# Performance work log

Hardware: AMD Instinct MI355X
Metric: run time of the kernel (lower is better)

## Reference

```python
import jax, jax.numpy as jnp
import numpy as np

B = 4
DIM = 512          # d_model
L = 4096           # n_tokens
D_STATE = 16
D_CONV = 4
EXPAND = 2
D_INNER = EXPAND * DIM          # 1024
DT_RANK = (DIM + 15) // 16      # ceil(dim/16) = 32
EPS = 1e-5


def setup_inputs() -> dict:
    key = jax.random.key(0)
    ks = jax.random.split(key, 8)
    s = 0.02
    A_log = jnp.log(jnp.tile(jnp.arange(1.0, D_STATE + 1.0, dtype=jnp.float32), (D_INNER, 1)))
    return {
        "x": jax.random.normal(ks[0], (B, DIM, L), jnp.float32),
        "ln_w": jnp.ones((DIM,), jnp.float32),
        "ln_b": jnp.zeros((DIM,), jnp.float32),
        "W_in": jax.random.normal(ks[1], (2 * D_INNER, DIM), jnp.float32) * s,
        "conv_w": jax.random.normal(ks[2], (D_INNER, 1, D_CONV), jnp.float32) * s,
        "conv_b": jnp.zeros((D_INNER,), jnp.float32),
        "W_xproj": jax.random.normal(ks[3], (DT_RANK + 2 * D_STATE, D_INNER), jnp.float32) * s,
        "W_dt": jax.random.normal(ks[4], (D_INNER, DT_RANK), jnp.float32) * s,
        "b_dt": jax.random.normal(ks[5], (D_INNER,), jnp.float32) * 0.1,
        "A_log": A_log,
        "D": jnp.ones((D_INNER,), jnp.float32),
        "W_out": jax.random.normal(ks[6], (DIM, D_INNER), jnp.float32) * s,
    }


def reference(x, ln_w, ln_b, W_in, conv_w, conv_b, W_xproj, W_dt, b_dt, A_log, D, W_out):
    Bsz = x.shape[0]
    # [B, d_model, L] -> [B, L, d_model]
    xt = jnp.swapaxes(x, 1, 2)
    # LayerNorm
    mu = jnp.mean(xt, axis=-1, keepdims=True)
    var = jnp.mean(jnp.square(xt - mu), axis=-1, keepdims=True)
    xn = (xt - mu) * jax.lax.rsqrt(var + EPS) * ln_w + ln_b
    # in_proj -> x, z branches
    xz = xn @ W_in.T                       # [B, L, 2*d_inner]
    xin, z = jnp.split(xz, 2, axis=-1)
    # causal depthwise conv1d (torch pads d_conv-1 both sides then truncates to L)
    xc = jnp.swapaxes(xin, 1, 2)           # [B, d_inner, L]
    xc = jax.lax.conv_general_dilated(
        xc, conv_w, window_strides=(1,), padding=[(D_CONV - 1, 0)],
        dimension_numbers=("NCH", "OIH", "NCH"), feature_group_count=D_INNER)
    xc = xc + conv_b[None, :, None]
    u = jax.nn.silu(jnp.swapaxes(xc, 1, 2))  # [B, L, d_inner]
    # input-dependent SSM parameters
    dbl = u @ W_xproj.T                    # [B, L, dt_rank + 2*d_state]
    dt = dbl[..., :DT_RANK]
    Bm = dbl[..., DT_RANK:DT_RANK + D_STATE]
    Cm = dbl[..., DT_RANK + D_STATE:]
    delta = jax.nn.softplus(dt @ W_dt.T + b_dt)  # [B, L, d_inner]
    A = -jnp.exp(A_log)                    # [d_inner, d_state]

    def step(h, inp):
        d_t, b_t, c_t, u_t = inp           # [B,di], [B,ds], [B,ds], [B,di]
        dA = jnp.exp(d_t[..., None] * A)   # [B, di, ds]
        h = dA * h + (d_t * u_t)[..., None] * b_t[:, None, :]
        y = jnp.einsum("bds,bs->bd", h, c_t)
        return h, y

    h0 = jnp.zeros((Bsz, D_INNER, D_STATE), x.dtype)
    xs = (jnp.swapaxes(delta, 0, 1), jnp.swapaxes(Bm, 0, 1),
          jnp.swapaxes(Cm, 0, 1), jnp.swapaxes(u, 0, 1))
    _, ys = jax.lax.scan(step, h0, xs)     # ys: [L, B, d_inner]
    y = jnp.swapaxes(ys, 0, 1) + u * D
    y = y * jax.nn.silu(z)
    out = y @ W_out.T                      # [B, L, d_model]
    return jnp.swapaxes(out, 1, 2)         # [B, d_model, L]
```

## Files before the change

### kernel.cpp

```cpp
#include <hip/hip_runtime.h>
#include <math.h>

#define Bsz 4
#define DIM 512
#define LEN 4096
#define DST 16
#define DIN 1024
#define NCH 64
#define CHL 64

typedef unsigned short ushort_t;
typedef unsigned int uint_t;
typedef __attribute__((ext_vector_type(8))) short short8;
typedef __attribute__((ext_vector_type(8))) unsigned short ushort8;
typedef __attribute__((ext_vector_type(8))) _Float16 half8;
typedef __attribute__((ext_vector_type(4))) float f32x4;

__device__ __forceinline__ float sigmoidf_(float x){ return 1.0f/(1.0f+__expf(-x)); }
__device__ __forceinline__ float bf2f(ushort_t u){ return __uint_as_float(((uint_t)u) << 16); }
__device__ __forceinline__ ushort_t f2bf(float f){
  uint_t x = __float_as_uint(f);
  uint_t r = (x + 0x7FFFu + ((x >> 16) & 1u)) >> 16;
  return (ushort_t)r;
}
__device__ __forceinline__ ushort_t f2h_bits(float f){
  _Float16 h = (_Float16)f;
  union { _Float16 h; ushort_t u; } v; v.h = h; return v.u;
}
__device__ __forceinline__ void gl2lds16(const void* g, void* l){
  __builtin_amdgcn_global_load_lds((const __attribute__((address_space(1))) void*)g,
                                   (__attribute__((address_space(3))) void*)l, 16, 0, 0);
}
#define POW_CHAIN(av, a1) \
  { float a2=a1*a1, a4=a2*a2, a8=a4*a4; \
    av[0]=a1; av[1]=a2; av[2]=a2*a1; av[3]=a4; \
    av[4]=a4*a1; av[5]=a4*a2; av[6]=a4*av[2]; av[7]=a8; \
    av[8]=a8*a1; av[9]=a8*a2; av[10]=a8*av[2]; av[11]=a8*a4; \
    av[12]=a8*av[4]; av[13]=a8*av[5]; av[14]=a8*av[6]; av[15]=a8*a8; }

__device__ __forceinline__ bool load_nA(const float* Alog, int d, float* nA){
  bool fast = true;
  #pragma unroll
  for(int s=0;s<DST;s++){
    float v = -__expf(Alog[d*DST+s]);
    float tgt = -(float)(s+1);
    if(fabsf(v - tgt) < 1e-4f*(float)(s+1)) v = tgt;
    else fast = false;
    nA[s] = v;
  }
  return fast;
}

__global__ __launch_bounds__(256) void ln_stats_k(const float* __restrict__ x,
                                                  float* __restrict__ mu, float* __restrict__ rs){
  int bid = blockIdx.x;
  int b = bid >> 6;
  int lg = bid & 63;
  int lane = threadIdx.x & 63;
  int g = threadIdx.x >> 6;
  int l = lg*64 + lane;
  const float* xb = x + (size_t)b*DIM*LEN + l;
  float s = 0.f, sq = 0.f;
  for(int d = g*128; d < g*128 + 128; ++d){
    float v = xb[(size_t)d*LEN];
    s += v; sq += v*v;
  }
  __shared__ float rsum[4][64], rsq[4][64];
  rsum[g][lane] = s; rsq[g][lane] = sq;
  __syncthreads();
  if(threadIdx.x < 64){
    float ts = 0.f, tq = 0.f;
    for(int gg=0; gg<4; ++gg){ ts += rsum[gg][lane]; tq += rsq[gg][lane]; }
    float m = ts * (1.0f/DIM);
    float var = tq * (1.0f/DIM) - m*m;
    mu[b*LEN + l] = m;
    rs[b*LEN + l] = rsqrtf(var + 1e-5f);
  }
}

__global__ __launch_bounds__(256) void wcvt_k(const float* __restrict__ Win,
    const float* __restrict__ Wout, const float* __restrict__ Wxp,
    ushort_t* __restrict__ Winb, ushort_t* __restrict__ Woutb, ushort_t* __restrict__ Wxpb){
  int i = blockIdx.x*256 + threadIdx.x;
  if(i < 1048576) Winb[i] = f2bf(Win[i]);
  else if(i < 1572864) Woutb[i-1048576] = f2bf(Wout[i-1048576]);
  else if(i < 1638400) Wxpb[i-1572864] = f2bf(Wxp[i-1572864]);
}

__global__ __launch_bounds__(256) void xnt_k(const float* __restrict__ x,
    const float* __restrict__ mu, const float* __restrict__ rs,
    const float* __restrict__ lnw, const float* __restrict__ lnb, ushort_t* __restrict__ xnT){
  __shared__ ushort_t t[64][72];
  int bid = blockIdx.x;
  int lt = bid & 63;
  int dt_ = (bid >> 6) & 7;
  int b = bid >> 9;
  int l0 = lt*64, d0 = dt_*64;
  int ll = threadIdx.x & 63;
  int dq = threadIdx.x >> 6;
  float mul_ = mu[b*LEN + l0 + ll], rsl = rs[b*LEN + l0 + ll];
  const float* xb = x + (size_t)b*DIM*LEN;
  #pragma unroll
  for(int i=0;i<16;i++){
    int d = d0 + dq*16 + i;
    float v = xb[(size_t)d*LEN + l0 + ll];
    t[ll][dq*16 + i] = f2bf((v - mul_)*rsl*lnw[d] + lnb[d]);
  }
  __syncthreads();
  int lr = threadIdx.x >> 2, seg = threadIdx.x & 3;
  ushort_t* dst = &xnT[(size_t)(b*LEN + l0 + lr)*DIM + d0 + seg*16];
  #pragma unroll
  for(int k=0;k<4;k++){
    ushort4 v = *(const ushort4*)&t[lr][seg*16 + k*4];
    *(ushort4*)&dst[k*4] = v;
  }
}

__global__ __launch_bounds__(256) void gemm1_mfma(const ushort_t* __restrict__ A,
    const ushort_t* __restrict__ Bw, _Float16* __restrict__ xin, ushort_t* __restrict__ sz){
  __shared__ __align__(16) ushort_t smem[2*16384];
  int tid = threadIdx.x;
  int wave = tid >> 6, lane = tid & 63;
  int flat = blockIdx.y * 16 + blockIdx.x;
  int orig = (flat & 7) * 256 + (flat >> 3);
  int n0 = (orig & 15) * 128;
  int m0 = (orig >> 4) * 128;
  int wm = (wave >> 1) * 64, wn = (wave & 1) * 64;
  int lm = lane & 15;
  int lk = lane >> 4;
  int sx = lm & 7;
  f32x4 zero4 = {0.f,0.f,0.f,0.f};
  f32x4 acc[4][4];
  #pragma unroll
  for(int i=0;i<4;i++)
    #pragma unroll
    for(int j=0;j<4;j++) acc[i][j] = zero4;
  #pragma unroll
  for(int i=0;i<4;i++){
    int c = i*256 + tid, r = c >> 3, kc = c & 7;
    int kg = kc ^ (r & 7);
    gl2lds16(&A [(size_t)(m0 + r)*512 + kg*8], &smem[c*8]);
    gl2lds16(&Bw[(size_t)(n0 + r)*512 + kg*8], &smem[8192 + c*8]);
  }
  int cur = 0;
  for(int t=0; t<8; ++t){
    if(t < 7){
      int k0n = (t+1)*64;
      ushort_t* Ad = &smem[(cur^1)*16384];
      ushort_t* Bd = &smem[(cur^1)*16384 + 8192];
      #pragma unroll
      for(int i=0;i<4;i++){
        int c = i*256 + tid, r = c >> 3, kc = c & 7;
        int kg = kc ^ (r & 7);
        gl2lds16(&A [(size_t)(m0 + r)*512 + k0n + kg*8], &Ad[c*8]);
        gl2lds16(&Bw[(size_t)(n0 + r)*512 + k0n + kg*8], &Bd[c*8]);
      }
      asm volatile("s_waitcnt vmcnt(8)" ::: "memory");
    } else {
      asm volatile("s_waitcnt vmcnt(0)" ::: "memory");
    }
    __builtin_amdgcn_sched_barrier(0);
    __builtin_amdgcn_s_barrier();
    const ushort_t* As = &smem[cur*16384];
    const ushort_t* Bs = &smem[cur*16384 + 8192];
    #pragma unroll
    for(int kk=0; kk<64; kk+=32){
      short8 af[4], bf[4];
      int ch = ((kk >> 3) + lk) ^ sx;
      #pragma unroll
      for(int i=0;i<4;i++){
        af[i] = *(const short8*)&As[(wm + i*16 + lm)*64 + ch*8];
        bf[i] = *(const short8*)&Bs[(wn + i*16 + lm)*64 + ch*8];
      }
      #pragma unroll
      for(int i=0;i<4;i++)
        #pragma unroll
        for(int j=0;j<4;j++)
          acc[i][j] = __builtin_amdgcn_mfma_f32_16x16x32_bf16(af[i], bf[j], acc[i][j], 0, 0, 0);
    }
    __builtin_amdgcn_s_barrier();
    cur ^= 1;
  }
  ushort_t* T = smem;
  bool is_z = (n0 >= 1024);
  #pragma unroll
  for(int i=0;i<4;i++)
    #pragma unroll
    for(int j=0;j<4;j++)
      #pragma unroll
      for(int r=0;r<4;r++){
        int ml = wm + i*16 + lk*4 + r;
        int nl = wn + j*16 + lm;
        float v = acc[i][j][r];
        T[ml*136 + nl] = is_z ? f2bf(v * sigmoidf_(v)) : f2h_bits(v);
      }
  __syncthreads();
  int rr = tid >> 4, cc = (tid & 15)*8;
  #pragma unroll
  for(int p=0;p<8;p++){
    int row = p*16 + rr;
    ushort8 v = *(const ushort8*)&T[row*136 + cc];
    if(!is_z) *(ushort8*)((ushort_t*)xin + (size_t)(m0+row)*DIN + n0 + cc) = v;
    else      *(ushort8*)&sz[(size_t)(m0+row)*DIN + (n0-1024) + cc] = v;
  }
}

__global__ __launch_bounds__(256) void conv_silu_k(const _Float16* __restrict__ xin,
    const float* __restrict__ cw, const float* __restrict__ cb, ushort_t* __restrict__ u){
  int idx = blockIdx.x*256 + threadIdx.x;
  int dg = idx & 127;
  int lc = (idx >> 7) & 511;
  int b  = idx >> 16;
  int d0 = dg*8;
  int l0 = lc*8;
  float bias[8];
  #pragma unroll
  for(int k=0;k<8;k+=4){
    float4 c4 = *(const float4*)&cb[d0+k];
    bias[k]=c4.x; bias[k+1]=c4.y; bias[k+2]=c4.z; bias[k+3]=c4.w;
  }
  float w[8][4];
  #pragma unroll
  for(int k=0;k<8;k++){
    float4 c4 = *(const float4*)&cw[(d0+k)*4];
    w[k][0]=c4.x; w[k][1]=c4.y; w[k][2]=c4.z; w[k][3]=c4.w;
  }
  const _Float16* base = xin + ((size_t)b*LEN)*DIN + d0;
  ushort_t* ub = u + ((size_t)b*LEN)*DIN + d0;
  float f0[8], f1[8], f2[8];
  if(lc > 0){
    half8 h0 = *(const half8*)&base[(size_t)(l0-3)*DIN];
    half8 h1 = *(const half8*)&base[(size_t)(l0-2)*DIN];
    half8 h2 = *(const half8*)&base[(size_t)(l0-1)*DIN];
    #pragma unroll
    for(int k=0;k<8;k++){ f0[k]=(float)h0[k]; f1[k]=(float)h1[k]; f2[k]=(float)h2[k]; }
  } else {
    #pragma unroll
    for(int k=0;k<8;k++){ f0[k]=0.f; f1[k]=0.f; f2[k]=0.f; }
  }
  #pragma unroll
  for(int t=0;t<8;t++){
    half8 xv = *(const half8*)&base[(size_t)(l0+t)*DIN];
    float f3[8];
    #pragma unroll
    for(int k=0;k<8;k++) f3[k] = (float)xv[k];
    short8 o;
    #pragma unroll
    for(int k=0;k<8;k++){
      float a = bias[k] + f0[k]*w[k][0] + f1[k]*w[k][1] + f2[k]*w[k][2] + f3[k]*w[k][3];
      float v = a * sigmoidf_(a);
      o[k] = (short)f2bf(v);
    }
    *(short8*)&ub[(size_t)(l0+t)*DIN] = o;
    #pragma unroll
    for(int k=0;k<8;k++){ f0[k]=f1[k]; f1[k]=f2[k]; f2[k]=f3[k]; }
  }
}

__global__ __launch_bounds__(256) void gemm2_mfma(const ushort_t* __restrict__ A,
    const ushort_t* __restrict__ Bw, float* __restrict__ dbl){
  __shared__ __align__(16) ushort_t smem[2*8192];
  int tid = threadIdx.x;
  int wave = tid >> 6, lane = tid & 63;
  int m0 = blockIdx.x * 64;
  int wm = (wave >> 1) * 32, wn = (wave & 1) * 32;
  int lm = lane & 15;
  int lk = lane >> 4;
  int sx = lm & 7;
  f32x4 zero4 = {0.f,0.f,0.f,0.f};
  f32x4 acc[2][2];
  #pragma unroll
  for(int i=0;i<2;i++){ acc[i][0] = zero4; acc[i][1] = zero4; }
  #pragma unroll
  for(int i=0;i<2;i++){
    int c = i*256 + tid, r = c >> 3, kc = c & 7;
    int kg = kc ^ (r & 7);
    gl2lds16(&A [(size_t)(m0 + r)*1024 + kg*8], &smem[c*8]);
    gl2lds16(&Bw[(size_t)r*1024 + kg*8], &smem[4096 + c*8]);
  }
  int cur = 0;
  for(int t=0; t<16; ++t){
    if(t < 15){
      int k0n = (t+1)*64;
      ushort_t* Ad = &smem[(cur^1)*8192];
      ushort_t* Bd = &smem[(cur^1)*8192 + 4096];
      #pragma unroll
      for(int i=0;i<2;i++){
        int c = i*256 + tid, r = c >> 3, kc = c & 7;
        int kg = kc ^ (r & 7);
        gl2lds16(&A [(size_t)(m0 + r)*1024 + k0n + kg*8], &Ad[c*8]);
        gl2lds16(&Bw[(size_t)r*1024 + k0n + kg*8], &Bd[c*8]);
      }
      asm volatile("s_waitcnt vmcnt(4)" ::: "memory");
    } else {
      asm volatile("s_waitcnt vmcnt(0)" ::: "memory");
    }
    __builtin_amdgcn_sched_barrier(0);
    __builtin_amdgcn_s_barrier();
    const ushort_t* As = &smem[cur*8192];
    const ushort_t* Bs = &smem[cur*8192 + 4096];
    #pragma unroll
    for(int kk=0; kk<64; kk+=32){
      short8 af[2], bf[2];
      int ch = ((kk >> 3) + lk) ^ sx;
      #pragma unroll
      for(int i=0;i<2;i++) af[i] = *(const short8*)&As[(wm + i*16 + lm)*64 + ch*8];
      #pragma unroll
      for(int j=0;j<2;j++) bf[j] = *(const short8*)&Bs[(wn + j*16 + lm)*64 + ch*8];
      #pragma unroll
      for(int i=0;i<2;i++)
        #pragma unroll
        for(int j=0;j<2;j++)
          acc[i][j] = __builtin_amdgcn_mfma_f32_16x16x32_bf16(af[i], bf[j], acc[i][j], 0, 0, 0);
    }
    __builtin_amdgcn_s_barrier();
    cur ^= 1;
  }
  #pragma unroll
  for(int i=0;i<2;i++)
    #pragma unroll
    for(int j=0;j<2;j++)
      #pragma unroll
      for(int r=0;r<4;r++){
        int m = m0 + wm + i*16 + lk*4 + r;
        int n = wn + j*16 + lm;
        dbl[(size_t)m*64 + n] = acc[i][j][r];
      }
}

__global__ __launch_bounds__(256,4) void deltag_k(const float* __restrict__ dbl,
    const float* __restrict__ Wdt, const float* __restrict__ bdt,
    _Float16* __restrict__ dF){
  __shared__ __align__(16) float dts[64*32];
  int bid = blockIdx.x;
  int d0 = (bid & 3) * 256;
  int m0 = (bid >> 2) * 64;
  int tid = threadIdx.x;
  const f32x4* src4 = (const f32x4*)(dbl + (size_t)m0*64);
  f32x4* dst4 = (f32x4*)dts;
  for(int i=tid; i<64*8; i+=256){
    int row = i >> 3, q = i & 7;
    dst4[i] = src4[row*16 + q];
  }
  int d = d0 + tid;
  float w[32];
  #pragma unroll
  for(int k=0;k<32;k+=4){
    float4 t4 = *(const float4*)&Wdt[d*32+k];
    w[k]=t4.x; w[k+1]=t4.y; w[k+2]=t4.z; w[k+3]=t4.w;
  }
  float bd = bdt[d];
  __syncthreads();
  for(int m=0;m<64;m++){
    const float* row = dts + m*32;
    float dtv = bd;
    #pragma unroll
    for(int k=0;k<32;k+=4){
      f32x4 q = *(const f32x4*)&row[k];
      dtv += q.x*w[k] + q.y*w[k+1] + q.z*w[k+2] + q.w*w[k+3];
    }
    float dv = dtv > 15.f ? dtv : __logf(1.f + __expf(dtv));
    dF[(size_t)(m0+m)*DIN + d] = (_Float16)dv;
  }
}

__global__ __launch_bounds__(256,4) void scanA_k(const ushort_t* __restrict__ u,
    const float* __restrict__ dbl, const float* __restrict__ Alog,
    const _Float16* __restrict__ dF,
    float* __restrict__ E, float* __restrict__ cum){
  __shared__ __align__(16) float dch[CHL*16];
  int bid = blockIdx.x;
  int c = bid & (NCH-1);
  int dblk = (bid >> 6) & 3;
  int b = bid >> 8;
  int d = dblk*256 + threadIdx.x;
  const f32x4* src = (const f32x4*)(dbl + ((size_t)b*LEN + c*CHL)*64);
  f32x4* dst4 = (f32x4*)dch;
  for(int i=threadIdx.x; i<CHL*4; i+=256){
    int t = i >> 2, q = i & 3;
    dst4[i] = src[t*16 + 8 + q];
  }
  float nA[DST];
  bool fast = load_nA(Alog, d, nA);
  float Es[DST];
  #pragma unroll
  for(int s=0;s<DST;s++) Es[s] = 0.f;
  float cumD = 0.f;
  __syncthreads();
  const ushort_t*  uu = u  + ((size_t)b*LEN + c*CHL)*DIN + d;
  const _Float16*  pd = dF + ((size_t)b*LEN + c*CHL)*DIN + d;
  if(fast){
    for(int t=0;t<CHL;++t){
      float dv = (float)pd[(size_t)t*DIN];
      float uv = bf2f(uu[(size_t)t*DIN]);
      float du = dv*uv;
      cumD += dv;
      float a1 = __expf(-dv);
      float av[DST];
      POW_CHAIN(av, a1);
      const f32x4* r4 = (const f32x4*)(dch + t*16);
      f32x4 B0=r4[0], B1=r4[1], B2=r4[2], B3=r4[3];
      Es[0]=av[0]*Es[0]+du*B0.x;  Es[1]=av[1]*Es[1]+du*B0.y;
      Es[2]=av[2]*Es[2]+du*B0.z;  Es[3]=av[3]*Es[3]+du*B0.w;
      Es[4]=av[4]*Es[4]+du*B1.x;  Es[5]=av[5]*Es[5]+du*B1.y;
      Es[6]=av[6]*Es[6]+du*B1.z;  Es[7]=av[7]*Es[7]+du*B1.w;
      Es[8]=av[8]*Es[8]+du*B2.x;  Es[9]=av[9]*Es[9]+du*B2.y;
      Es[10]=av[10]*Es[10]+du*B2.z; Es[11]=av[11]*Es[11]+du*B2.w;
      Es[12]=av[12]*Es[12]+du*B3.x; Es[13]=av[13]*Es[13]+du*B3.y;
      Es[14]=av[14]*Es[14]+du*B3.z; Es[15]=av[15]*Es[15]+du*B3.w;
    }
  } else {
    for(int t=0;t<CHL;++t){
      float dv = (float)pd[(size_t)t*DIN];
      float uv = bf2f(uu[(size_t)t*DIN]);
      float du = dv*uv;
      cumD += dv;
      const float* row = dch + t*16;
      #pragma unroll
      for(int s=0;s<DST;s++){
        float a = __expf(dv*nA[s]);
        Es[s] = a*Es[s] + du*row[s];
      }
    }
  }
  size_t o = (size_t)(b*NCH + c)*DST*DIN + d;
  #pragma unroll
  for(int s=0;s<DST;s++) E[o + (size_t)s*DIN] = Es[s];
  cum[(size_t)(b*NCH + c)*DIN + d] = cumD;
}

__global__ __launch_bounds__(256) void scanB_k(const float* __restrict__ cum,
    const float* __restrict__ Alog, float* __restrict__ E){
  int g = blockIdx.x*256 + threadIdx.x;
  int d = g & 1023;
  int s = (g >> 10) & 15;
  int b = g >> 14;
  float v = -__expf(Alog[d*DST + s]);
  float tgt = -(float)(s+1);
  float nA = (fabsf(v - tgt) < 1e-4f*(float)(s+1)) ? tgt : v;
  float h = 0.f;
  for(int c=0;c<NCH;c++){
    float p = __expf(cum[(size_t)(b*NCH + c)*DIN + d] * nA);
    size_t o = (size_t)((b*NCH + c)*DST + s)*DIN + d;
    float e = E[o];
    E[o] = h;
    h = p*h + e;
  }
}

__global__ __launch_bounds__(256,4) void scanC_k(ushort_t* __restrict__ u,
    const float* __restrict__ dbl, const float* __restrict__ Alog,
    const float* __restrict__ Hs, const float* __restrict__ Dp, const ushort_t* __restrict__ sz,
    const _Float16* __restrict__ dF){
  __shared__ __align__(16) float dch[CHL*32];
  int bid = blockIdx.x;
  int c = bid & (NCH-1);
  int dblk = (bid >> 6) & 3;
  int b = bid >> 8;
  int d = dblk*256 + threadIdx.x;
  const f32x4* src = (const f32x4*)(dbl + ((size_t)b*LEN + c*CHL)*64);
  f32x4* dst4 = (f32x4*)dch;
  for(int i=threadIdx.x; i<CHL*8; i+=256){
    int t = i >> 3, q = i & 7;
    dst4[i] = src[t*16 + 8 + q];
  }
  float nA[DST];
  bool fast = load_nA(Alog, d, nA);
  float h[DST];
  size_t ho = (size_t)(b*NCH + c)*DST*DIN + d;
  #pragma unroll
  for(int s=0;s<DST;s++) h[s] = Hs[ho + (size_t)s*DIN];
  float Dv = Dp[d];
  __syncthreads();
  ushort_t* uu = u + ((size_t)b*LEN + c*CHL)*DIN + d;
  const ushort_t* zz = sz + ((size_t)b*LEN + c*CHL)*DIN + d;
  const _Float16* pd = dF + ((size_t)b*LEN + c*CHL)*DIN + d;
  if(fast){
    for(int t=0;t<CHL;++t){
      float dv = (float)pd[(size_t)t*DIN];
      float uv = bf2f(uu[(size_t)t*DIN]);
      float du = dv*uv;
      float a1 = __expf(-dv);
      float av[DST];
      POW_CHAIN(av, a1);
      const f32x4* r4 = (const f32x4*)(dch + t*32);
      f32x4 B0=r4[0], B1=r4[1], B2=r4[2], B3=r4[3];
      f32x4 C0=r4[4], C1=r4[5], C2=r4[6], C3=r4[7];
      float y0, y1, y2, y3;
      h[0]=av[0]*h[0]+du*B0.x;  h[1]=av[1]*h[1]+du*B0.y;
      h[2]=av[2]*h[2]+du*B0.z;  h[3]=av[3]*h[3]+du*B0.w;
      y0 = h[0]*C0.x + h[1]*C0.y; y1 = h[2]*C0.z + h[3]*C0.w;
      h[4]=av[4]*h[4]+du*B1.x;  h[5]=av[5]*h[5]+du*B1.y;
      h[6]=av[6]*h[6]+du*B1.z;  h[7]=av[7]*h[7]+du*B1.w;
      y2 = h[4]*C1.x + h[5]*C1.y; y3 = h[6]*C1.z + h[7]*C1.w;
      h[8]=av[8]*h[8]+du*B2.x;  h[9]=av[9]*h[9]+du*B2.y;
      h[10]=av[10]*h[10]+du*B2.z; h[11]=av[11]*h[11]+du*B2.w;
      y0 += h[8]*C2.x + h[9]*C2.y; y1 += h[10]*C2.z + h[11]*C2.w;
      h[12]=av[12]*h[12]+du*B3.x; h[13]=av[13]*h[13]+du*B3.y;
      h[14]=av[14]*h[14]+du*B3.z; h[15]=av[15]*h[15]+du*B3.w;
      y2 += h[12]*C3.x + h[13]*C3.y; y3 += h[14]*C3.z + h[15]*C3.w;
      float y = (y0+y1) + (y2+y3) + uv*Dv;
      y *= bf2f(zz[(size_t)t*DIN]);
      uu[(size_t)t*DIN] = f2bf(y);
    }
  } else {
    for(int t=0;t<CHL;++t){
      float dv = (float)pd[(size_t)t*DIN];
      float uv = bf2f(uu[(size_t)t*DIN]);
      float du = dv*uv;
      const float* row = dch + t*32;
      float y = 0.f;
      #pragma unroll
      for(int s=0;s<DST;s++){
        float a = __expf(dv*nA[s]);
        h[s] = a*h[s] + du*row[s];
        y += h[s]*row[16+s];
      }
      y += uv*Dv;
      y *= bf2f(zz[(size_t)t*DIN]);
      uu[(size_t)t*DIN] = f2bf(y);
    }
  }
}

__global__ __launch_bounds__(256) void gemm4_mfma(const ushort_t* __restrict__ A,
    const ushort_t* __restrict__ Bw, float* __restrict__ out){
  __shared__ __align__(16) ushort_t smem[2*16384];
  int tid = threadIdx.x;
  int wave = tid >> 6, lane = tid & 63;
  int flat = blockIdx.y * 4 + blockIdx.x;
  int orig = (flat & 7) * 64 + (flat >> 3);
  int n0 = (orig & 3) * 128;
  int m0 = (orig >> 2) * 128;
  int wm = (wave >> 1) * 64, wn = (wave & 1) * 64;
  int lm = lane & 15;
  int lk = lane >> 4;
  int sx = lm & 7;
  f32x4 zero4 = {0.f,0.f,0.f,0.f};
  f32x4 acc[4][4];
  #pragma unroll
  for(int i=0;i<4;i++)
    #pragma unroll
    for(int j=0;j<4;j++) acc[i][j] = zero4;
  #pragma unroll
  for(int i=0;i<4;i++){
    int c = i*256 + tid, r = c >> 3, kc = c & 7;
    int kg = kc ^ (r & 7);
    gl2lds16(&A [(size_t)(m0 + r)*1024 + kg*8], &smem[c*8]);
    gl2lds16(&Bw[(size_t)(n0 + r)*1024 + kg*8], &smem[8192 + c*8]);
  }
  int cur = 0;
  for(int t=0; t<16; ++t){
    if(t < 15){
      int k0n = (t+1)*64;
      ushort_t* Ad = &smem[(cur^1)*16384];
      ushort_t* Bd = &smem[(cur^1)*16384 + 8192];
      #pragma unroll
      for(int i=0;i<4;i++){
        int c = i*256 + tid, r = c >> 3, kc = c & 7;
        int kg = kc ^ (r & 7);
        gl2lds16(&A [(size_t)(m0 + r)*1024 + k0n + kg*8], &Ad[c*8]);
        gl2lds16(&Bw[(size_t)(n0 + r)*1024 + k0n + kg*8], &Bd[c*8]);
      }
      asm volatile("s_waitcnt vmcnt(8)" ::: "memory");
    } else {
      asm volatile("s_waitcnt vmcnt(0)" ::: "memory");
    }
    __builtin_amdgcn_sched_barrier(0);
    __builtin_amdgcn_s_barrier();
    const ushort_t* As = &smem[cur*16384];
    const ushort_t* Bs = &smem[cur*16384 + 8192];
    #pragma unroll
    for(int kk=0; kk<64; kk+=32){
      short8 af[4], bf[4];
      int ch = ((kk >> 3) + lk) ^ sx;
      #pragma unroll
      for(int i=0;i<4;i++){
        af[i] = *(const short8*)&As[(wm + i*16 + lm)*64 + ch*8];
        bf[i] = *(const short8*)&Bs[(wn + i*16 + lm)*64 + ch*8];
      }
      #pragma unroll
      for(int i=0;i<4;i++)
        #pragma unroll
        for(int j=0;j<4;j++)
          acc[i][j] = __builtin_amdgcn_mfma_f32_16x16x32_bf16(af[i], bf[j], acc[i][j], 0, 0, 0);
    }
    __builtin_amdgcn_s_barrier();
    cur ^= 1;
  }
  float* T = (float*)smem;
  int b = m0 >> 12, l0 = m0 & 4095;
  for(int g=0; g<4; ++g){
    __syncthreads();
    if((g >> 1) == (wave & 1)){
      int jg = g & 1;
      #pragma unroll
      for(int j2=0;j2<2;j2++){
        int j = jg*2 + j2;
        #pragma unroll
        for(int i=0;i<4;i++)
          #pragma unroll
          for(int r=0;r<4;r++){
            int ml = wm + i*16 + lk*4 + r;
            int nl = wn + j*16 + lm - g*32;
            T[nl*132 + ml] = acc[i][j][r];
          }
      }
    }
    __syncthreads();
    int nl = tid >> 3, seg = tid & 7;
    float* dst = &out[((size_t)b*DIM + n0 + g*32 + nl)*LEN + l0 + seg*16];
    #pragma unroll
    for(int k=0;k<4;k++){
      float4 v = *(const float4*)&T[nl*132 + seg*16 + k*4];
      *(float4*)&dst[k*4] = v;
    }
  }
}

extern "C" void kernel_launch(void* const* d_in, const int* in_sizes, int n_in,
                              void* d_out, int out_size, void* d_ws, size_t ws_size,
                              hipStream_t stream) {
  const float* x    = (const float*)d_in[0];
  const float* lnw  = (const float*)d_in[1];
  const float* lnb  = (const float*)d_in[2];
  const float* Win  = (const float*)d_in[3];
  const float* cw   = (const float*)d_in[4];
  const float* cb   = (const float*)d_in[5];
  const float* Wxp  = (const float*)d_in[6];
  const float* Wdt  = (const float*)d_in[7];
  const float* bdt  = (const float*)d_in[8];
  const float* Alog = (const float*)d_in[9];
  const float* Dp   = (const float*)d_in[10];
  const float* Wout = (const float*)d_in[11];
  float* out = (float*)d_out;
  float* ws  = (float*)d_ws;

  float*    mu   = ws;
  float*    rs   = ws + 16384;
  _Float16* xin  = (_Float16*)(ws + 32768);
  _Float16* dF   = (_Float16*)(ws + 32768);
  float*    E    = ws + 32768 + 8388608;
  float*    cum  = ws + 32768 + 12582912;
  ushort_t* sz   = (ushort_t*)(ws + 32768 + 16777216);
  ushort_t* u    = (ushort_t*)(ws + 32768 + 16777216 + 8388608);
  ushort_t* xnT  = (ushort_t*)(ws + 32768 + 16777216 + 16777216);
  float*    dbl  = (float*)xnT;
  ushort_t* Winb = (ushort_t*)(ws + 32768 + 16777216 + 16777216 + 4194304);
  ushort_t* Woutb= Winb + 1048576;
  ushort_t* Wxpb = Woutb + 524288;

  hipLaunchKernelGGL(ln_stats_k, dim3(256),     dim3(256), 0, stream, x, mu, rs);
  hipLaunchKernelGGL(wcvt_k,     dim3(6400),    dim3(256), 0, stream, Win, Wout, Wxp, Winb, Woutb, Wxpb);
  hipLaunchKernelGGL(xnt_k,      dim3(2048),    dim3(256), 0, stream, x, mu, rs, lnw, lnb, xnT);
  hipLaunchKernelGGL(gemm1_mfma, dim3(16,128),  dim3(256), 0, stream, xnT, Winb, xin, sz);
  hipLaunchKernelGGL(conv_silu_k,dim3(1024),    dim3(256), 0, stream, xin, cw, cb, u);
  hipLaunchKernelGGL(gemm2_mfma, dim3(256),     dim3(256), 0, stream, u, Wxpb, dbl);
  hipLaunchKernelGGL(deltag_k,   dim3(1024),    dim3(256), 0, stream, dbl, Wdt, bdt, dF);
  hipLaunchKernelGGL(scanA_k,    dim3(1024),    dim3(256), 0, stream, u, dbl, Alog, dF, E, cum);
  hipLaunchKernelGGL(scanB_k,    dim3(256),     dim3(256), 0, stream, cum, Alog, E);
  hipLaunchKernelGGL(scanC_k,    dim3(1024),    dim3(256), 0, stream, u, dbl, Alog, E, Dp, sz, dF);
  hipLaunchKernelGGL(gemm4_mfma, dim3(4,128),   dim3(256), 0, stream, u, Woutb, out);
}
```

Measured before the change: 353.7 us.

## Enlarge GEMM tiles to 256x128 with 512 threads and triple-buffered LDS

Both MFMA GEMMs (in_proj and out_proj) now use 256x128 block tiles computed by eight waves instead of 128x128 by four waves. LDS loading changes from a double-buffered to a three-stage pipeline, with vmcnt waits adjusted to match. The aim is better reuse of B-operand tiles, fewer blocks and deeper latency hiding of global loads. The cost is 144KB of shared memory per block, which limits each CU to one block and lowers occupancy. The epilogues are reworked to write out in two halves or with wider transpose rows.

```diff
diff --git a/kernel.cpp b/kernel.cpp
--- a/kernel.cpp
+++ b/kernel.cpp
@@ -116,15 +116,15 @@
   }
 }
 
-__global__ __launch_bounds__(256) void gemm1_mfma(const ushort_t* __restrict__ A,
+__global__ __launch_bounds__(512) void gemm1_mfma(const ushort_t* __restrict__ A,
     const ushort_t* __restrict__ Bw, _Float16* __restrict__ xin, ushort_t* __restrict__ sz){
-  __shared__ __align__(16) ushort_t smem[2*16384];
+  __shared__ __align__(16) ushort_t smem[3*24576];
   int tid = threadIdx.x;
   int wave = tid >> 6, lane = tid & 63;
-  int flat = blockIdx.y * 16 + blockIdx.x;
-  int orig = (flat & 7) * 256 + (flat >> 3);
+  int flat = blockIdx.x;
+  int orig = (flat & 7) * 128 + (flat >> 3);
   int n0 = (orig & 15) * 128;
-  int m0 = (orig >> 4) * 128;
+  int m0 = (orig >> 4) * 256;
   int wm = (wave >> 1) * 64, wn = (wave & 1) * 64;
   int lm = lane & 15;
   int lk = lane >> 4;
@@ -135,34 +135,37 @@
   for(int i=0;i<4;i++)
     #pragma unroll
     for(int j=0;j<4;j++) acc[i][j] = zero4;
-  #pragma unroll
-  for(int i=0;i<4;i++){
-    int c = i*256 + tid, r = c >> 3, kc = c & 7;
-    int kg = kc ^ (r & 7);
-    gl2lds16(&A [(size_t)(m0 + r)*512 + kg*8], &smem[c*8]);
-    gl2lds16(&Bw[(size_t)(n0 + r)*512 + kg*8], &smem[8192 + c*8]);
-  }
-  int cur = 0;
-  for(int t=0; t<8; ++t){
-    if(t < 7){
-      int k0n = (t+1)*64;
-      ushort_t* Ad = &smem[(cur^1)*16384];
-      ushort_t* Bd = &smem[(cur^1)*16384 + 8192];
-      #pragma unroll
-      for(int i=0;i<4;i++){
-        int c = i*256 + tid, r = c >> 3, kc = c & 7;
-        int kg = kc ^ (r & 7);
-        gl2lds16(&A [(size_t)(m0 + r)*512 + k0n + kg*8], &Ad[c*8]);
-        gl2lds16(&Bw[(size_t)(n0 + r)*512 + k0n + kg*8], &Bd[c*8]);
-      }
-      asm volatile("s_waitcnt vmcnt(8)" ::: "memory");
-    } else {
-      asm volatile("s_waitcnt vmcnt(0)" ::: "memory");
-    }
+
+  auto STAGE = [&](int kt, int bi){
+    int k0 = kt*64;
+    ushort_t* As = &smem[bi*24576];
+    ushort_t* Bs = &smem[bi*24576 + 16384];
+    #pragma unroll
+    for(int i=0;i<4;i++){
+      int c = i*512 + tid, r = c >> 3, kc = c & 7;
+      int kg = kc ^ (r & 7);
+      gl2lds16(&A[(size_t)(m0 + r)*512 + k0 + kg*8], &As[c*8]);
+    }
+    #pragma unroll
+    for(int i=0;i<2;i++){
+      int c = i*512 + tid, r = c >> 3, kc = c & 7;
+      int kg = kc ^ (r & 7);
+      gl2lds16(&Bw[(size_t)(n0 + r)*512 + k0 + kg*8], &Bs[c*8]);
+    }
+  };
+
+  STAGE(0, 0);
+  STAGE(1, 1);
+  for(int kt=0; kt<8; ++kt){
+    int bi = kt % 3;
+    if(kt + 2 < 8) STAGE(kt+2, (kt+2) % 3);
+    if(kt < 6)       asm volatile("s_waitcnt vmcnt(12)" ::: "memory");
+    else if(kt == 6) asm volatile("s_waitcnt vmcnt(6)"  ::: "memory");
+    else             asm volatile("s_waitcnt vmcnt(0)"  ::: "memory");
     __builtin_amdgcn_sched_barrier(0);
     __builtin_amdgcn_s_barrier();
-    const ushort_t* As = &smem[cur*16384];
-    const ushort_t* Bs = &smem[cur*16384 + 8192];
+    const ushort_t* As = &smem[bi*24576];
+    const ushort_t* Bs = &smem[bi*24576 + 16384];
     #pragma unroll
     for(int kk=0; kk<64; kk+=32){
       short8 af[4], bf[4];
@@ -179,29 +182,34 @@
           acc[i][j] = __builtin_amdgcn_mfma_f32_16x16x32_bf16(af[i], bf[j], acc[i][j], 0, 0, 0);
     }
     __builtin_amdgcn_s_barrier();
-    cur ^= 1;
   }
   ushort_t* T = smem;
   bool is_z = (n0 >= 1024);
-  #pragma unroll
-  for(int i=0;i<4;i++)
-    #pragma unroll
-    for(int j=0;j<4;j++)
-      #pragma unroll
-      for(int r=0;r<4;r++){
-        int ml = wm + i*16 + lk*4 + r;
-        int nl = wn + j*16 + lm;
-        float v = acc[i][j][r];
-        T[ml*136 + nl] = is_z ? f2bf(v * sigmoidf_(v)) : f2h_bits(v);
-      }
-  __syncthreads();
-  int rr = tid >> 4, cc = (tid & 15)*8;
-  #pragma unroll
-  for(int p=0;p<8;p++){
-    int row = p*16 + rr;
-    ushort8 v = *(const ushort8*)&T[row*136 + cc];
-    if(!is_z) *(ushort8*)((ushort_t*)xin + (size_t)(m0+row)*DIN + n0 + cc) = v;
-    else      *(ushort8*)&sz[(size_t)(m0+row)*DIN + (n0-1024) + cc] = v;
+  for(int h=0; h<2; ++h){
+    __syncthreads();
+    if((wave >> 2) == h){
+      #pragma unroll
+      for(int i=0;i<4;i++)
+        #pragma unroll
+        for(int j=0;j<4;j++)
+          #pragma unroll
+          for(int r=0;r<4;r++){
+            int ml = (wm - h*128) + i*16 + lk*4 + r;
+            int nl = wn + j*16 + lm;
+            float v = acc[i][j][r];
+            T[ml*136 + nl] = is_z ? f2bf(v * sigmoidf_(v)) : f2h_bits(v);
+          }
+    }
+    __syncthreads();
+    int rr = tid >> 4, cc = (tid & 15)*8;
+    #pragma unroll
+    for(int p=0;p<4;p++){
+      int row = p*32 + rr;
+      ushort8 v = *(const ushort8*)&T[row*136 + cc];
+      int gm = m0 + h*128 + row;
+      if(!is_z) *(ushort8*)((ushort_t*)xin + (size_t)gm*DIN + n0 + cc) = v;
+      else      *(ushort8*)&sz[(size_t)gm*DIN + (n0-1024) + cc] = v;
+    }
   }
 }
 
@@ -523,15 +531,15 @@
   }
 }
 
-__global__ __launch_bounds__(256) void gemm4_mfma(const ushort_t* __restrict__ A,
+__global__ __launch_bounds__(512) void gemm4_mfma(const ushort_t* __restrict__ A,
     const ushort_t* __restrict__ Bw, float* __restrict__ out){
-  __shared__ __align__(16) ushort_t smem[2*16384];
+  __shared__ __align__(16) ushort_t smem[3*24576];
   int tid = threadIdx.x;
   int wave = tid >> 6, lane = tid & 63;
-  int flat = blockIdx.y * 4 + blockIdx.x;
-  int orig = (flat & 7) * 64 + (flat >> 3);
+  int flat = blockIdx.x;
+  int orig = (flat & 7) * 32 + (flat >> 3);
   int n0 = (orig & 3) * 128;
-  int m0 = (orig >> 2) * 128;
+  int m0 = (orig >> 2) * 256;
   int wm = (wave >> 1) * 64, wn = (wave & 1) * 64;
   int lm = lane & 15;
   int lk = lane >> 4;
@@ -542,34 +550,37 @@
   for(int i=0;i<4;i++)
     #pragma unroll
     for(int j=0;j<4;j++) acc[i][j] = zero4;
-  #pragma unroll
-  for(int i=0;i<4;i++){
-    int c = i*256 + tid, r = c >> 3, kc = c & 7;
-    int kg = kc ^ (r & 7);
-    gl2lds16(&A [(size_t)(m0 + r)*1024 + kg*8], &smem[c*8]);
-    gl2lds16(&Bw[(size_t)(n0 + r)*1024 + kg*8], &smem[8192 + c*8]);
-  }
-  int cur = 0;
-  for(int t=0; t<16; ++t){
-    if(t < 15){
-      int k0n = (t+1)*64;
-      ushort_t* Ad = &smem[(cur^1)*16384];
-      ushort_t* Bd = &smem[(cur^1)*16384 + 8192];
-      #pragma unroll
-      for(int i=0;i<4;i++){
-        int c = i*256 + tid, r = c >> 3, kc = c & 7;
-        int kg = kc ^ (r & 7);
-        gl2lds16(&A [(size_t)(m0 + r)*1024 + k0n + kg*8], &Ad[c*8]);
-        gl2lds16(&Bw[(size_t)(n0 + r)*1024 + k0n + kg*8], &Bd[c*8]);
-      }
-      asm volatile("s_waitcnt vmcnt(8)" ::: "memory");
-    } else {
-      asm volatile("s_waitcnt vmcnt(0)" ::: "memory");
-    }
+
+  auto STAGE = [&](int kt, int bi){
+    int k0 = kt*64;
+    ushort_t* As = &smem[bi*24576];
+    ushort_t* Bs = &smem[bi*24576 + 16384];
+    #pragma unroll
+    for(int i=0;i<4;i++){
+      int c = i*512 + tid, r = c >> 3, kc = c & 7;
+      int kg = kc ^ (r & 7);
+      gl2lds16(&A[(size_t)(m0 + r)*1024 + k0 + kg*8], &As[c*8]);
+    }
+    #pragma unroll
+    for(int i=0;i<2;i++){
+      int c = i*512 + tid, r = c >> 3, kc = c & 7;
+      int kg = kc ^ (r & 7);
+      gl2lds16(&Bw[(size_t)(n0 + r)*1024 + k0 + kg*8], &Bs[c*8]);
+    }
+  };
+
+  STAGE(0, 0);
+  STAGE(1, 1);
+  for(int kt=0; kt<16; ++kt){
+    int bi = kt % 3;
+    if(kt + 2 < 16) STAGE(kt+2, (kt+2) % 3);
+    if(kt < 14)       asm volatile("s_waitcnt vmcnt(12)" ::: "memory");
+    else if(kt == 14) asm volatile("s_waitcnt vmcnt(6)"  ::: "memory");
+    else              asm volatile("s_waitcnt vmcnt(0)"  ::: "memory");
     __builtin_amdgcn_sched_barrier(0);
     __builtin_amdgcn_s_barrier();
-    const ushort_t* As = &smem[cur*16384];
-    const ushort_t* Bs = &smem[cur*16384 + 8192];
+    const ushort_t* As = &smem[bi*24576];
+    const ushort_t* Bs = &smem[bi*24576 + 16384];
     #pragma unroll
     for(int kk=0; kk<64; kk+=32){
       short8 af[4], bf[4];
@@ -586,13 +597,12 @@
           acc[i][j] = __builtin_amdgcn_mfma_f32_16x16x32_bf16(af[i], bf[j], acc[i][j], 0, 0, 0);
     }
     __builtin_amdgcn_s_barrier();
-    cur ^= 1;
   }
   float* T = (float*)smem;
   int b = m0 >> 12, l0 = m0 & 4095;
   for(int g=0; g<4; ++g){
     __syncthreads();
-    if((g >> 1) == (wave & 1)){
+    if((wave & 1) == (g >> 1)){
       int jg = g & 1;
       #pragma unroll
       for(int j2=0;j2<2;j2++){
@@ -603,16 +613,16 @@
           for(int r=0;r<4;r++){
             int ml = wm + i*16 + lk*4 + r;
             int nl = wn + j*16 + lm - g*32;
-            T[nl*132 + ml] = acc[i][j][r];
+            T[nl*264 + ml] = acc[i][j][r];
           }
       }
     }
     __syncthreads();
-    int nl = tid >> 3, seg = tid & 7;
+    int nl = tid >> 4, seg = tid & 15;
     float* dst = &out[((size_t)b*DIM + n0 + g*32 + nl)*LEN + l0 + seg*16];
     #pragma unroll
     for(int k=0;k<4;k++){
-      float4 v = *(const float4*)&T[nl*132 + seg*16 + k*4];
+      float4 v = *(const float4*)&T[nl*264 + seg*16 + k*4];
       *(float4*)&dst[k*4] = v;
     }
   }
@@ -653,12 +663,12 @@
   hipLaunchKernelGGL(ln_stats_k, dim3(256),     dim3(256), 0, stream, x, mu, rs);
   hipLaunchKernelGGL(wcvt_k,     dim3(6400),    dim3(256), 0, stream, Win, Wout, Wxp, Winb, Woutb, Wxpb);
   hipLaunchKernelGGL(xnt_k,      dim3(2048),    dim3(256), 0, stream, x, mu, rs, lnw, lnb, xnT);
-  hipLaunchKernelGGL(gemm1_mfma, dim3(16,128),  dim3(256), 0, stream, xnT, Winb, xin, sz);
+  hipLaunchKernelGGL(gemm1_mfma, dim3(1024),    dim3(512), 0, stream, xnT, Winb, xin, sz);
   hipLaunchKernelGGL(conv_silu_k,dim3(1024),    dim3(256), 0, stream, xin, cw, cb, u);
   hipLaunchKernelGGL(gemm2_mfma, dim3(256),     dim3(256), 0, stream, u, Wxpb, dbl);
   hipLaunchKernelGGL(deltag_k,   dim3(1024),    dim3(256), 0, stream, dbl, Wdt, bdt, dF);
   hipLaunchKernelGGL(scanA_k,    dim3(1024),    dim3(256), 0, stream, u, dbl, Alog, dF, E, cum);
   hipLaunchKernelGGL(scanB_k,    dim3(256),     dim3(256), 0, stream, cum, Alog, E);
   hipLaunchKernelGGL(scanC_k,    dim3(1024),    dim3(256), 0, stream, u, dbl, Alog, E, Dp, sz, dF);
-  hipLaunchKernelGGL(gemm4_mfma, dim3(4,128),   dim3(256), 0, stream, u, Woutb, out);
-}
+  hipLaunchKernelGGL(gemm4_mfma, dim3(256),     dim3(512), 0, stream, u, Woutb, out);
+}
```

New measurement: 370.2 us. 1.05x slower.
